# Performance work log

Measured on AMD Instinct MI355X. Metric: run time of the kernel, lower is better.

The kernel has to match this reference:

```python
import jax, jax.numpy as jnp
import numpy as np

B, T, C = 4, 2048, 1024
NH = 16
HD = C // NH


def setup_inputs() -> dict:
    key = jax.random.key(0)
    k1, k2, k3 = jax.random.split(key, 3)
    x = jax.random.normal(k1, (B, T, C), dtype=jnp.float32)
    Wqkv = jax.random.normal(k2, (C, 3 * C), dtype=jnp.float32) * 0.02
    bqkv = jnp.zeros((3 * C,), dtype=jnp.float32)
    Wproj = jax.random.normal(k3, (C, C), dtype=jnp.float32) * 0.02
    bproj = jnp.zeros((C,), dtype=jnp.float32)
    return {"x": x, "Wqkv": Wqkv, "bqkv": bqkv, "Wproj": Wproj, "bproj": bproj}


def reference(x, Wqkv, bqkv, Wproj, bproj):
    Bx, Tx, Cx = x.shape
    qkv = x @ Wqkv + bqkv  # [B,T,3C]
    q, k, v = jnp.split(qkv, 3, axis=-1)
    # [B, NH, T, HD]
    q = q.reshape(Bx, Tx, NH, HD).transpose(0, 2, 1, 3)
    k = k.reshape(Bx, Tx, NH, HD).transpose(0, 2, 1, 3)
    v = v.reshape(Bx, Tx, NH, HD).transpose(0, 2, 1, 3)
    scale = 1.0 / jnp.sqrt(jnp.float32(HD))
    att = jnp.einsum('bhqd,bhkd->bhqk', q, k) * scale  # [B,NH,T,T]
    causal = jnp.tril(jnp.ones((Tx, Tx), dtype=bool))
    att = jnp.where(causal, att, jnp.float32(-jnp.inf))
    att = jax.nn.softmax(att, axis=-1)
    y = jnp.einsum('bhqk,bhkd->bhqd', att, v)  # [B,NH,T,HD]
    y = y.transpose(0, 2, 1, 3).reshape(Bx, Tx, Cx)
    return y @ Wproj + bproj
```

## Files before the change

kernel.cpp:

```cpp
#include <hip/hip_runtime.h>
#include <hip/hip_bf16.h>
#include <math.h>

#define B_  4
#define T_  2048
#define C_  1024
#define NH_ 16
#define HD_ 64

using bf16 = __hip_bfloat16;
typedef __attribute__((ext_vector_type(8))) short bf16x8;
typedef __attribute__((ext_vector_type(4))) short bf16x4;
typedef __attribute__((ext_vector_type(4))) float f32x4;

__device__ __forceinline__ bf16 f2b(float f){ return __float2bfloat16(f); }

__device__ __forceinline__ short f2bs(float f){
  union { float f; unsigned u; } x; x.f = f;
  x.u += 0x7FFFu + ((x.u >> 16) & 1u);
  return (short)(x.u >> 16);
}

__device__ __forceinline__ bf16x4 pack_bf16x4(float a, float b, float c, float d){
  union { bf16x4 v; __hip_bfloat162 h[2]; } u;
  u.h[0] = __float22bfloat162_rn(make_float2(a, b));
  u.h[1] = __float22bfloat162_rn(make_float2(c, d));
  return u.v;
}

__device__ __forceinline__ void async_load16(const bf16* g, bf16* l){
  __builtin_amdgcn_global_load_lds((const __attribute__((address_space(1))) unsigned int*)g,
                                   (__attribute__((address_space(3))) unsigned int*)l,
                                   16, 0, 0);
}

#define QSCALE 0.18033688011112042f

__global__ __launch_bounds__(256) void k_prep(const float* __restrict__ x, bf16* __restrict__ xb, int n,
                                              const float* __restrict__ in0, bf16* __restrict__ out0,
                                              const float* __restrict__ in1, bf16* __restrict__ out1){
  __shared__ float t[32][33];
  int b = blockIdx.x;
  if (b < 8192){
    int i = (b * 256 + threadIdx.x) * 4;
    if (i < n){
      float4 f = *(const float4*)(x + i);
      ushort4 u;
      u.x = (unsigned short)f2bs(f.x);
      u.y = (unsigned short)f2bs(f.y);
      u.z = (unsigned short)f2bs(f.z);
      u.w = (unsigned short)f2bs(f.w);
      *(ushort4*)(xb + i) = u;
    }
    return;
  }
  b -= 8192;
  const float* in; bf16* out; int Cc, bx, by;
  if (b < 3072){ in = in0; out = out0; Cc = 3*C_; bx = (b % 96)*32; by = (b / 96)*32; }
  else { b -= 3072; in = in1; out = out1; Cc = C_; bx = (b & 31)*32; by = (b >> 5)*32; }
  const int R = C_;
  int lx = threadIdx.x & 31, ly = threadIdx.x >> 5;
  #pragma unroll
  for (int s = 0; s < 4; s++){
    int k = by + ly + s*8;
    t[ly + s*8][lx] = in[(size_t)k * Cc + bx + lx];
  }
  __syncthreads();
  #pragma unroll
  for (int s = 0; s < 4; s++){
    int n2 = bx + ly + s*8;
    out[(size_t)n2 * R + by + lx] = f2b(t[lx][ly + s*8]);
  }
}

template<int MODE, int BM>
__global__ __launch_bounds__(BM*2) void k_gemm(
    const bf16* __restrict__ A, const bf16* __restrict__ BT,
    const float* __restrict__ bias,
    bf16* __restrict__ qo, bf16* __restrict__ ko, bf16* __restrict__ vo,
    float* __restrict__ fout,
    int M, int N, int K)
{
  constexpr int NTHR = BM*2;
  constexpr int WMW  = BM/64;
  constexpr int NB   = 512/NTHR;
  __shared__ bf16 As[3][BM*32];
  __shared__ bf16 Bs[3][128*32];

  const int tid  = threadIdx.x;
  const int wave = tid >> 6, lane = tid & 63;
  const int wm = wave % WMW, wn = wave / WMW;
  const int quad = lane >> 4, l15 = lane & 15;
  const int bm = blockIdx.x * BM;
  const int bn = blockIdx.y * 128;

  const bf16* gA[2]; bf16* lA[2];
  #pragma unroll
  for (int s = 0; s < 2; s++){
    const int c = tid + s*NTHR;
    const int r = c >> 2, p = (c & 3) ^ ((r >> 1) & 3);
    gA[s] = A + (size_t)(bm + r)*K + p*8;
    lA[s] = &As[0][0] + (size_t)c*8;
  }
  const bf16* gB[NB]; bf16* lB[NB];
  #pragma unroll
  for (int s = 0; s < NB; s++){
    const int c = tid + s*NTHR;
    const int r = c >> 2, p = (c & 3) ^ ((r >> 1) & 3);
    gB[s] = BT + (size_t)(bn + r)*K + p*8;
    lB[s] = &Bs[0][0] + (size_t)c*8;
  }
  const int fsw = (l15 >> 1) & 3;

  f32x4 acc[4][4] = {};
  const int nK = K >> 5;

  #pragma unroll
  for (int s = 0; s < 2; s++) async_load16(gA[s], lA[s]);
  #pragma unroll
  for (int s = 0; s < NB; s++) async_load16(gB[s], lB[s]);
  #pragma unroll
  for (int s = 0; s < 2; s++) async_load16(gA[s] + 32, lA[s] + BM*32);
  #pragma unroll
  for (int s = 0; s < NB; s++) async_load16(gB[s] + 32, lB[s] + 128*32);

  for (int kt = 0; kt < nK; kt++){
    if (kt + 1 < nK){
      if constexpr (NB == 1) asm volatile("s_waitcnt vmcnt(3)" ::: "memory");
      else                   asm volatile("s_waitcnt vmcnt(4)" ::: "memory");
    } else {
      asm volatile("s_waitcnt vmcnt(0)" ::: "memory");
    }
    __builtin_amdgcn_s_barrier();
    __builtin_amdgcn_sched_barrier(0);

    if (kt + 2 < nK){
      const int off = (kt + 2) * 32;
      const int bi  = (kt + 2) % 3;
      const int ba  = bi * (BM*32);
      const int bb  = bi * 4096;
      #pragma unroll
      for (int s = 0; s < 2; s++) async_load16(gA[s] + off, lA[s] + ba);
      #pragma unroll
      for (int s = 0; s < NB; s++) async_load16(gB[s] + off, lB[s] + bb);
    }
    const bf16* as = &As[kt % 3][0];
    const bf16* bs = &Bs[kt % 3][0];

    bf16x8 af[4], bfv[4];
    #pragma unroll
    for (int i = 0; i < 4; i++)
      af[i]  = *reinterpret_cast<const bf16x8*>(as + (wm*64 + i*16 + l15)*32 + ((quad ^ fsw) << 3));
    #pragma unroll
    for (int j = 0; j < 4; j++)
      bfv[j] = *reinterpret_cast<const bf16x8*>(bs + (wn*64 + j*16 + l15)*32 + ((quad ^ fsw) << 3));
    #pragma unroll
    for (int i = 0; i < 4; i++)
      #pragma unroll
      for (int j = 0; j < 4; j++)
        acc[i][j] = __builtin_amdgcn_mfma_f32_16x16x32_bf16(af[i], bfv[j], acc[i][j], 0, 0, 0);
  }

  if (MODE == 0){
    const int sec = bn >> 10;
    const int bb2 = bm >> 11;
    const int tb  = (bm & (T_ - 1)) + wm*64 + quad*4;
    const int hn  = ((bn & 1023) >> 6) + wn;
    const size_t bhx = (size_t)(bb2 * NH_ + hn);
    if (sec == 2){
      #pragma unroll
      for (int j = 0; j < 4; j++){
        const int d = j*16 + l15;
        const float bj = bias[bn + wn*64 + j*16 + l15];
        bf16* vrow = vo + (bhx * HD_ + d) * (size_t)T_;
        const int sw = (l15 & 7) * 8;
        #pragma unroll
        for (int i = 0; i < 4; i++){
          const int t = (tb + i*16) ^ sw;
          *reinterpret_cast<bf16x4*>(vrow + t) =
            pack_bf16x4(acc[i][j][0] + bj, acc[i][j][1] + bj,
                        acc[i][j][2] + bj, acc[i][j][3] + bj);
        }
      }
    } else {
      bf16* dst = (sec == 0) ? qo : ko;
      const float sc = (sec == 0) ? QSCALE : 1.0f;
      #pragma unroll
      for (int j = 0; j < 4; j++){
        const int d = j*16 + l15;
        const float bj = bias[bn + wn*64 + j*16 + l15];
        bf16* base = dst + bhx * T_ * HD_;
        #pragma unroll
        for (int i = 0; i < 4; i++){
          const int t0 = tb + i*16;
          #pragma unroll
          for (int r = 0; r < 4; r++){
            const int dq = d ^ (((quad*4 + r) & 7) * 8);
            short s = f2bs((acc[i][j][r] + bj) * sc);
            base[(size_t)(t0 + r) * HD_ + dq] = *(bf16*)&s;
          }
        }
      }
    }
  } else {
    #pragma unroll
    for (int i = 0; i < 4; i++){
      #pragma unroll
      for (int j = 0; j < 4; j++){
        const int n = bn + wn*64 + j*16 + l15;
        const float bj = bias[n];
        float* p0 = fout + (size_t)(bm + wm*64 + i*16 + quad*4) * N + n;
        #pragma unroll
        for (int r = 0; r < 4; r++)
          p0[(size_t)r * N] = acc[i][j][r] + bj;
      }
    }
  }
}

__global__ __launch_bounds__(256) void k_attn(
    const bf16* __restrict__ Q, const bf16* __restrict__ Kg,
    const bf16* __restrict__ Vt, bf16* __restrict__ Y)
{
  __shared__ bf16 Ks[2][64*64];
  __shared__ bf16 Vs[2][64*64];

  const int bh = blockIdx.x;
  const int bb = bh >> 4, hh = bh & 15;
  const int qt = 15 - blockIdx.y;
  const int tid  = threadIdx.x;
  const int wave = tid >> 6, lane = tid & 63;
  const int quad = lane >> 4, l15 = lane & 15;
  const int swz  = (l15 & 7) * 8;

  const size_t baseQK = (size_t)bh * T_ * HD_;
  const size_t baseV  = (size_t)bh * HD_ * T_;

  const int ca = wave, cb = wave + 4;
  const bf16* kg_a = Kg + baseQK + ca*512 + (size_t)lane*8;
  const bf16* kg_b = Kg + baseQK + cb*512 + (size_t)lane*8;
  const bf16* vg_a = Vt + baseV + (size_t)(ca*8 + (lane>>3)) * T_ + (lane&7)*8;
  const bf16* vg_b = Vt + baseV + (size_t)(cb*8 + (lane>>3)) * T_ + (lane&7)*8;
  bf16* kl_a0 = &Ks[0][0] + ca*512;  bf16* kl_b0 = &Ks[0][0] + cb*512;
  bf16* vl_a0 = &Vs[0][0] + ca*512;  bf16* vl_b0 = &Vs[0][0] + cb*512;

  bf16x4 ones_f;
  {
    short v = (l15 == 0) ? f2bs(1.0f) : (short)0;
    ones_f = (bf16x4){ v, v, v, v };
  }

  const int jmax = 2*qt + 1;

  bf16x8 qf[2][2];
  #pragma unroll
  for (int s = 0; s < 2; s++){
    const int t = qt*128 + s*64 + wave*16 + l15;
    #pragma unroll
    for (int ks = 0; ks < 2; ks++){
      const int col = (ks*32 + quad*8) ^ swz;
      qf[s][ks] = *reinterpret_cast<const bf16x8*>(Q + baseQK + (size_t)t*HD_ + col);
    }
  }

  async_load16(kg_a, kl_a0);  async_load16(kg_b, kl_b0);
  async_load16(vg_a, vl_a0);  async_load16(vg_b, vl_b0);

  f32x4 o[2][5] = {};

  for (int j = 0; j <= jmax; j++){
    __syncthreads();

    if (j < jmax){
      const int nb = ((j+1) & 1) * 4096;
      const size_t ko = (size_t)(j+1) * 64 * HD_;
      async_load16(kg_a + ko, kl_a0 + nb);  async_load16(kg_b + ko, kl_b0 + nb);
      async_load16(vg_a + (j+1)*64, vl_a0 + nb);
      async_load16(vg_b + (j+1)*64, vl_b0 + nb);
    }

    const bf16* ksb = &Ks[j & 1][0];
    const bf16* vsb = &Vs[j & 1][0];

    f32x4 st[2][4] = {};
    __builtin_amdgcn_s_setprio(1);
    #pragma unroll
    for (int ks = 0; ks < 2; ks++){
      #pragma unroll
      for (int tk = 0; tk < 4; tk++){
        bf16x8 kf = *reinterpret_cast<const bf16x8*>(ksb + (tk*16 + l15)*64 + ((ks*32 + quad*8) ^ swz));
        st[0][tk] = __builtin_amdgcn_mfma_f32_16x16x32_bf16(kf, qf[0][ks], st[0][tk], 0, 0, 0);
        st[1][tk] = __builtin_amdgcn_mfma_f32_16x16x32_bf16(kf, qf[1][ks], st[1][tk], 0, 0, 0);
      }
    }
    __builtin_amdgcn_s_setprio(0);

    bf16x4 pf[2][4];
    #pragma unroll
    for (int s = 0; s < 2; s++){
      const int qg = qt*128 + s*64 + wave*16 + l15;
      const bool msk = s ? (j > 2*qt) : (j >= 2*qt);
      #pragma unroll
      for (int tk = 0; tk < 4; tk++){
        float e[4];
        #pragma unroll
        for (int r = 0; r < 4; r++){
          float sv = st[s][tk][r];
          if (msk){
            const int kvg = j*64 + tk*16 + quad*4 + r;
            if (kvg > qg) sv = -1e30f;
          }
          e[r] = exp2f(sv);
        }
        pf[s][tk] = pack_bf16x4(e[0], e[1], e[2], e[3]);
      }
    }

    __builtin_amdgcn_s_setprio(1);
    #pragma unroll
    for (int td = 0; td < 4; td++){
      #pragma unroll
      for (int tk = 0; tk < 4; tk++){
        bf16x4 vf = *reinterpret_cast<const bf16x4*>(vsb + (td*16 + l15)*64 + ((tk*16 + quad*4) ^ swz));
        o[0][td] = __builtin_amdgcn_mfma_f32_16x16x16bf16_1k(vf, pf[0][tk], o[0][td], 0, 0, 0);
        o[1][td] = __builtin_amdgcn_mfma_f32_16x16x16bf16_1k(vf, pf[1][tk], o[1][td], 0, 0, 0);
      }
    }
    #pragma unroll
    for (int tk = 0; tk < 4; tk++){
      o[0][4] = __builtin_amdgcn_mfma_f32_16x16x16bf16_1k(ones_f, pf[0][tk], o[0][4], 0, 0, 0);
      o[1][4] = __builtin_amdgcn_mfma_f32_16x16x16bf16_1k(ones_f, pf[1][tk], o[1][4], 0, 0, 0);
    }
    __builtin_amdgcn_s_setprio(0);
  }

  #pragma unroll
  for (int s = 0; s < 2; s++){
    const float l = __shfl(o[s][4][0], l15, 64);
    const float inv = 1.0f / l;
    const int t = qt*128 + s*64 + wave*16 + l15;
    bf16* yrow = Y + ((size_t)(bb * T_ + t)) * C_ + hh * HD_;
    #pragma unroll
    for (int td = 0; td < 4; td++){
      *reinterpret_cast<bf16x4*>(yrow + td*16 + quad*4) =
        pack_bf16x4(o[s][td][0] * inv, o[s][td][1] * inv,
                    o[s][td][2] * inv, o[s][td][3] * inv);
    }
  }
}


extern "C" void kernel_launch(void* const* d_in, const int* in_sizes, int n_in,
                              void* d_out, int out_size, void* d_ws, size_t ws_size,
                              hipStream_t stream) {
  const float* x     = (const float*)d_in[0];
  const float* Wqkv  = (const float*)d_in[1];
  const float* bqkv  = (const float*)d_in[2];
  const float* Wproj = (const float*)d_in[3];
  const float* bproj = (const float*)d_in[4];
  float* out = (float*)d_out;

  const size_t M = (size_t)B_ * T_;
  char* w = (char*)d_ws;
  bf16* xb     = (bf16*)w;  w += M * C_ * 2;
  bf16* WqkvT  = (bf16*)w;  w += (size_t)3 * C_ * C_ * 2;
  bf16* WprojT = (bf16*)w;  w += (size_t)C_ * C_ * 2;
  bf16* Qb     = (bf16*)w;  w += M * C_ * 2;
  bf16* Kb     = (bf16*)w;  w += M * C_ * 2;
  bf16* Vtb    = (bf16*)w;  w += M * C_ * 2;
  bf16* Yb     = (bf16*)w;  w += M * C_ * 2;

  {
    int n = (int)(M * C_);
    k_prep<<<dim3(12288), dim3(256), 0, stream>>>(x, xb, n, Wqkv, WqkvT, Wproj, WprojT);
  }
  k_gemm<0,256><<<dim3(M/256, (3*C_)/128), dim3(512), 0, stream>>>(
      xb, WqkvT, bqkv, Qb, Kb, Vtb, nullptr, (int)M, 3*C_, C_);
  k_attn<<<dim3(64, 16), dim3(256), 0, stream>>>(Qb, Kb, Vtb, Yb);
  k_gemm<1,128><<<dim3(M/128, C_/128), dim3(256), 0, stream>>>(
      Yb, WprojT, bproj, nullptr, nullptr, nullptr, out, (int)M, C_, C_);
}
```

Baseline: 265.2 us.

## Use 256x256 GEMM tiles with double-buffered LDS and MFMA priority boosts

Replaces the templated GEMM with a single 256x256-tile kernel of 8 waves, where each wave computes 128x64 in two half-passes. Buffering drops from triple to double, with one prefetch per iteration and a full vmcnt(0) wait. s_setprio is raised around the MFMA blocks. The goal is more data reuse per LDS byte and fewer redundant global loads. The trade-offs are higher register pressure (acc[8][4]), a shallower pipeline, and fewer blocks for the output projection: 128 instead of 512 on 256 CUs, which risks underutilisation.

Measured after the change: 296.6 us. +11.8%, slower.

```diff
diff --git a/kernel.cpp b/kernel.cpp
--- a/kernel.cpp
+++ b/kernel.cpp
@@ -73,98 +73,102 @@
   }
 }
 
-template<int MODE, int BM>
-__global__ __launch_bounds__(BM*2) void k_gemm(
+template<int MODE>
+__global__ __launch_bounds__(512, 2) void k_gemm256(
     const bf16* __restrict__ A, const bf16* __restrict__ BT,
     const float* __restrict__ bias,
     bf16* __restrict__ qo, bf16* __restrict__ ko, bf16* __restrict__ vo,
     float* __restrict__ fout,
     int M, int N, int K)
 {
-  constexpr int NTHR = BM*2;
-  constexpr int WMW  = BM/64;
-  constexpr int NB   = 512/NTHR;
-  __shared__ bf16 As[3][BM*32];
-  __shared__ bf16 Bs[3][128*32];
+  __shared__ bf16 As[2][256*32];
+  __shared__ bf16 Bs[2][256*32];
 
   const int tid  = threadIdx.x;
   const int wave = tid >> 6, lane = tid & 63;
-  const int wm = wave % WMW, wn = wave / WMW;
+  const int wm = wave >> 2, wn = wave & 3;
   const int quad = lane >> 4, l15 = lane & 15;
-  const int bm = blockIdx.x * BM;
-  const int bn = blockIdx.y * 128;
-
-  const bf16* gA[2]; bf16* lA[2];
+  const int bm = blockIdx.x * 256;
+  const int bn = blockIdx.y * 256;
+
+  const bf16* gA[2]; const bf16* gB[2]; bf16* lA[2]; bf16* lB[2];
   #pragma unroll
   for (int s = 0; s < 2; s++){
-    const int c = tid + s*NTHR;
+    const int c = tid + s*512;
     const int r = c >> 2, p = (c & 3) ^ ((r >> 1) & 3);
-    gA[s] = A + (size_t)(bm + r)*K + p*8;
+    gA[s] = A  + (size_t)(bm + r)*K + p*8;
+    gB[s] = BT + (size_t)(bn + r)*K + p*8;
     lA[s] = &As[0][0] + (size_t)c*8;
-  }
-  const bf16* gB[NB]; bf16* lB[NB];
-  #pragma unroll
-  for (int s = 0; s < NB; s++){
-    const int c = tid + s*NTHR;
-    const int r = c >> 2, p = (c & 3) ^ ((r >> 1) & 3);
-    gB[s] = BT + (size_t)(bn + r)*K + p*8;
     lB[s] = &Bs[0][0] + (size_t)c*8;
   }
   const int fsw = (l15 >> 1) & 3;
 
-  f32x4 acc[4][4] = {};
-  const int nK = K >> 5;
-
-  #pragma unroll
-  for (int s = 0; s < 2; s++) async_load16(gA[s], lA[s]);
-  #pragma unroll
-  for (int s = 0; s < NB; s++) async_load16(gB[s], lB[s]);
-  #pragma unroll
-  for (int s = 0; s < 2; s++) async_load16(gA[s] + 32, lA[s] + BM*32);
-  #pragma unroll
-  for (int s = 0; s < NB; s++) async_load16(gB[s] + 32, lB[s] + 128*32);
-
-  for (int kt = 0; kt < nK; kt++){
-    if (kt + 1 < nK){
-      if constexpr (NB == 1) asm volatile("s_waitcnt vmcnt(3)" ::: "memory");
-      else                   asm volatile("s_waitcnt vmcnt(4)" ::: "memory");
-    } else {
-      asm volatile("s_waitcnt vmcnt(0)" ::: "memory");
+  f32x4 acc[8][4] = {};
+  const int nT = K >> 5;
+
+  #pragma unroll
+  for (int s = 0; s < 2; s++){ async_load16(gA[s], lA[s]); async_load16(gB[s], lB[s]); }
+  asm volatile("s_waitcnt vmcnt(0)" ::: "memory");
+  __builtin_amdgcn_s_barrier();
+  __builtin_amdgcn_sched_barrier(0);
+
+  for (int u = 0; u < nT; u++){
+    const bf16* as = &As[u & 1][0];
+    const bf16* bs = &Bs[u & 1][0];
+
+    if (u + 1 < nT){
+      const int off = (u + 1) * 32;
+      const int bo  = ((u + 1) & 1) * 8192;
+      #pragma unroll
+      for (int s = 0; s < 2; s++){
+        async_load16(gA[s] + off, lA[s] + bo);
+        async_load16(gB[s] + off, lB[s] + bo);
+      }
+    }
+    bf16x8 bfv[4];
+    #pragma unroll
+    for (int j = 0; j < 4; j++)
+      bfv[j] = *reinterpret_cast<const bf16x8*>(bs + (wn*64 + j*16 + l15)*32 + ((quad ^ fsw) << 3));
+    {
+      bf16x8 af[4];
+      #pragma unroll
+      for (int i = 0; i < 4; i++)
+        af[i] = *reinterpret_cast<const bf16x8*>(as + (wm*128 + i*16 + l15)*32 + ((quad ^ fsw) << 3));
+      __builtin_amdgcn_s_setprio(1);
+      #pragma unroll
+      for (int i = 0; i < 4; i++)
+        #pragma unroll
+        for (int j = 0; j < 4; j++)
+          acc[i][j] = __builtin_amdgcn_mfma_f32_16x16x32_bf16(af[i], bfv[j], acc[i][j], 0, 0, 0);
+      __builtin_amdgcn_s_setprio(0);
     }
     __builtin_amdgcn_s_barrier();
     __builtin_amdgcn_sched_barrier(0);
 
-    if (kt + 2 < nK){
-      const int off = (kt + 2) * 32;
-      const int bi  = (kt + 2) % 3;
-      const int ba  = bi * (BM*32);
-      const int bb  = bi * 4096;
-      #pragma unroll
-      for (int s = 0; s < 2; s++) async_load16(gA[s] + off, lA[s] + ba);
-      #pragma unroll
-      for (int s = 0; s < NB; s++) async_load16(gB[s] + off, lB[s] + bb);
-    }
-    const bf16* as = &As[kt % 3][0];
-    const bf16* bs = &Bs[kt % 3][0];
-
-    bf16x8 af[4], bfv[4];
-    #pragma unroll
-    for (int i = 0; i < 4; i++)
-      af[i]  = *reinterpret_cast<const bf16x8*>(as + (wm*64 + i*16 + l15)*32 + ((quad ^ fsw) << 3));
-    #pragma unroll
-    for (int j = 0; j < 4; j++)
-      bfv[j] = *reinterpret_cast<const bf16x8*>(bs + (wn*64 + j*16 + l15)*32 + ((quad ^ fsw) << 3));
-    #pragma unroll
-    for (int i = 0; i < 4; i++)
-      #pragma unroll
-      for (int j = 0; j < 4; j++)
-        acc[i][j] = __builtin_amdgcn_mfma_f32_16x16x32_bf16(af[i], bfv[j], acc[i][j], 0, 0, 0);
+    {
+      bf16x8 af[4];
+      #pragma unroll
+      for (int i = 0; i < 4; i++)
+        af[i] = *reinterpret_cast<const bf16x8*>(as + (wm*128 + (i+4)*16 + l15)*32 + ((quad ^ fsw) << 3));
+      __builtin_amdgcn_s_setprio(1);
+      #pragma unroll
+      for (int i = 0; i < 4; i++)
+        #pragma unroll
+        for (int j = 0; j < 4; j++)
+          acc[i+4][j] = __builtin_amdgcn_mfma_f32_16x16x32_bf16(af[i], bfv[j], acc[i+4][j], 0, 0, 0);
+      __builtin_amdgcn_s_setprio(0);
+    }
+    if (u + 1 < nT){
+      asm volatile("s_waitcnt vmcnt(0)" ::: "memory");
+      __builtin_amdgcn_s_barrier();
+      __builtin_amdgcn_sched_barrier(0);
+    }
   }
 
   if (MODE == 0){
     const int sec = bn >> 10;
     const int bb2 = bm >> 11;
-    const int tb  = (bm & (T_ - 1)) + wm*64 + quad*4;
+    const int tb  = (bm & (T_ - 1)) + wm*128 + quad*4;
     const int hn  = ((bn & 1023) >> 6) + wn;
     const size_t bhx = (size_t)(bb2 * NH_ + hn);
     if (sec == 2){
@@ -175,7 +179,7 @@
         bf16* vrow = vo + (bhx * HD_ + d) * (size_t)T_;
         const int sw = (l15 & 7) * 8;
         #pragma unroll
-        for (int i = 0; i < 4; i++){
+        for (int i = 0; i < 8; i++){
           const int t = (tb + i*16) ^ sw;
           *reinterpret_cast<bf16x4*>(vrow + t) =
             pack_bf16x4(acc[i][j][0] + bj, acc[i][j][1] + bj,
@@ -191,7 +195,7 @@
         const float bj = bias[bn + wn*64 + j*16 + l15];
         bf16* base = dst + bhx * T_ * HD_;
         #pragma unroll
-        for (int i = 0; i < 4; i++){
+        for (int i = 0; i < 8; i++){
           const int t0 = tb + i*16;
           #pragma unroll
           for (int r = 0; r < 4; r++){
@@ -204,12 +208,12 @@
     }
   } else {
     #pragma unroll
-    for (int i = 0; i < 4; i++){
+    for (int i = 0; i < 8; i++){
       #pragma unroll
       for (int j = 0; j < 4; j++){
         const int n = bn + wn*64 + j*16 + l15;
         const float bj = bias[n];
-        float* p0 = fout + (size_t)(bm + wm*64 + i*16 + quad*4) * N + n;
+        float* p0 = fout + (size_t)(bm + wm*128 + i*16 + quad*4) * N + n;
         #pragma unroll
         for (int r = 0; r < 4; r++)
           p0[(size_t)r * N] = acc[i][j][r] + bj;
@@ -374,9 +378,9 @@
     int n = (int)(M * C_);
     k_prep<<<dim3(12288), dim3(256), 0, stream>>>(x, xb, n, Wqkv, WqkvT, Wproj, WprojT);
   }
-  k_gemm<0,256><<<dim3(M/256, (3*C_)/128), dim3(512), 0, stream>>>(
+  k_gemm256<0><<<dim3(M/256, (3*C_)/256), dim3(512), 0, stream>>>(
       xb, WqkvT, bqkv, Qb, Kb, Vtb, nullptr, (int)M, 3*C_, C_);
   k_attn<<<dim3(64, 16), dim3(256), 0, stream>>>(Qb, Kb, Vtb, Yb);
-  k_gemm<1,128><<<dim3(M/128, C_/128), dim3(256), 0, stream>>>(
+  k_gemm256<1><<<dim3(M/256, C_/256), dim3(512), 0, stream>>>(
       Yb, WprojT, bproj, nullptr, nullptr, nullptr, out, (int)M, C_, C_);
 }
```
